# Kernel optimization log

Measured on AMD Instinct MI355X. Metric: run time of the kernel, lower is better.

Reference implementation:

```python
import jax, jax.numpy as jnp
import numpy as np

BS, N, D_IN, HID, D_OUT = 16, 256, 128, 128, 128


def setup_inputs() -> dict:
    key = jax.random.key(0)
    ks = jax.random.split(key, 10)
    s = 0.02
    return {
        "x": jax.random.normal(ks[0], (BS, N, D_IN), dtype=jnp.float32),
        "adj": jax.random.randint(ks[1], (BS, N, N), 0, 2, dtype=jnp.int32),
        "W_fc": jax.random.normal(ks[2], (D_IN, HID), dtype=jnp.float32) * s,
        "b_fc": jnp.zeros((HID,), dtype=jnp.float32),
        "W_a1": jax.random.normal(ks[3], (2 * HID, HID), dtype=jnp.float32) * s,
        "b_a1": jnp.zeros((HID,), dtype=jnp.float32),
        "w_a2": jax.random.normal(ks[4], (HID,), dtype=jnp.float32) * s,
        "b_a2": jnp.zeros((), dtype=jnp.float32),
        "W_out": jax.random.normal(ks[5], (HID, D_OUT), dtype=jnp.float32) * s,
        "b_out": jnp.zeros((D_OUT,), dtype=jnp.float32),
    }


def reference(x, adj, W_fc, b_fc, W_a1, b_a1, w_a2, b_a2, W_out, b_out):
    # h = fc(x): (bs, n, hid)
    h = jnp.einsum("bnd,dh->bnh", x, W_fc) + b_fc
    # attn first layer on concat([h_i, h_j]) decomposes into two half-projections
    # (same math as Linear(2*hid, hid) on the concatenated pair features).
    a_i = jnp.einsum("bnh,hk->bnk", h, W_a1[:HID])  # contribution of h_i
    a_j = jnp.einsum("bnh,hk->bnk", h, W_a1[HID:])  # contribution of h_j
    pre = a_i[:, :, None, :] + a_j[:, None, :, :] + b_a1  # (bs, n, n, hid)
    e = jnp.einsum("bijk,k->bij", jax.nn.relu(pre), w_a2) + b_a2  # (bs, n, n)
    e = jnp.where(adj == 0, jnp.float32(-1e9), e)
    attn = jax.nn.softmax(e, axis=-1)
    h_prime = jnp.einsum("bij,bjh->bih", attn, h)
    out = jnp.einsum("bih,ho->bio", h_prime, W_out) + b_out
    return out
```

## Files before the change

### kernel.cpp

```cpp
#include <hip/hip_runtime.h>

#define BS  16
#define NN  256
#define HID 128

__device__ __forceinline__ int xcd_swz(int bid) {
    return (bid & 7) * 128 + (bid >> 3);
}

__global__ __launch_bounds__(256, 4) void gat_k1(
    const float* __restrict__ x, const float* __restrict__ W_fc,
    const float* __restrict__ b_fc, const float* __restrict__ W_a1,
    const float* __restrict__ b_a1, const float* __restrict__ W_out,
    float* __restrict__ aiT, float* __restrict__ ajT, float* __restrict__ g)
{
    __shared__ __align__(16) float hs[4 * HID];

    const int tid = threadIdx.x;
    const int k   = tid & 127;
    const int q   = tid >> 7;
    const int swz = xcd_swz(blockIdx.x);
    const int r0  = swz * 4;
    const int b   = r0 >> 8;
    const int n0  = r0 & 255;

    const float* x0 = x + __builtin_amdgcn_readfirstlane((r0 + 2 * q) * HID);
    const float* x1 = x0 + HID;

    {
        const float bf = b_fc[k];
        float a0a = bf, a0b = 0.f, a1a = bf, a1b = 0.f;
        #pragma unroll 4
        for (int d0 = 0; d0 < HID; d0 += 8) {
            float w[8];
            #pragma unroll
            for (int t = 0; t < 8; ++t) w[t] = W_fc[(d0 + t) * HID + k];
            a0a += x0[d0+0]*w[0] + x0[d0+1]*w[1] + x0[d0+2]*w[2] + x0[d0+3]*w[3];
            a0b += x0[d0+4]*w[4] + x0[d0+5]*w[5] + x0[d0+6]*w[6] + x0[d0+7]*w[7];
            a1a += x1[d0+0]*w[0] + x1[d0+1]*w[1] + x1[d0+2]*w[2] + x1[d0+3]*w[3];
            a1b += x1[d0+4]*w[4] + x1[d0+5]*w[5] + x1[d0+6]*w[6] + x1[d0+7]*w[7];
        }
        hs[(2 * q + 0) * HID + k] = a0a + a0b;
        hs[(2 * q + 1) * HID + k] = a1a + a1b;
    }
    __syncthreads();

    {
        const float* Wp  = W_a1 + q * HID * HID;
        const float bias = q ? 0.f : b_a1[k];
        float acc[4][2];
        #pragma unroll
        for (int r = 0; r < 4; ++r) { acc[r][0] = bias; acc[r][1] = 0.f; }
        #pragma unroll 2
        for (int d0 = 0; d0 < HID; d0 += 8) {
            float w[8];
            #pragma unroll
            for (int t = 0; t < 8; ++t) w[t] = Wp[(d0 + t) * HID + k];
            #pragma unroll
            for (int r = 0; r < 4; ++r) {
                const float4 h0 = *(const float4*)&hs[r * HID + d0];
                const float4 h1 = *(const float4*)&hs[r * HID + d0 + 4];
                acc[r][0] += h0.x * w[0] + h0.y * w[1] + h0.z * w[2] + h0.w * w[3];
                acc[r][1] += h1.x * w[4] + h1.y * w[5] + h1.z * w[6] + h1.w * w[7];
            }
        }
        float* dst = (q ? ajT : aiT) + (b * HID + k) * NN + n0;
        const float4 v = {acc[0][0] + acc[0][1], acc[1][0] + acc[1][1],
                          acc[2][0] + acc[2][1], acc[3][0] + acc[3][1]};
        *(float4*)dst = v;
    }

    {
        float a0a = 0.f, a0b = 0.f, a1a = 0.f, a1b = 0.f;
        #pragma unroll 4
        for (int d0 = 0; d0 < HID; d0 += 8) {
            float w[8];
            #pragma unroll
            for (int t = 0; t < 8; ++t) w[t] = W_out[(d0 + t) * HID + k];
            const float4 hA0 = *(const float4*)&hs[(2 * q + 0) * HID + d0];
            const float4 hA1 = *(const float4*)&hs[(2 * q + 0) * HID + d0 + 4];
            const float4 hB0 = *(const float4*)&hs[(2 * q + 1) * HID + d0];
            const float4 hB1 = *(const float4*)&hs[(2 * q + 1) * HID + d0 + 4];
            a0a += hA0.x * w[0] + hA0.y * w[1] + hA0.z * w[2] + hA0.w * w[3];
            a0b += hA1.x * w[4] + hA1.y * w[5] + hA1.z * w[6] + hA1.w * w[7];
            a1a += hB0.x * w[0] + hB0.y * w[1] + hB0.z * w[2] + hB0.w * w[3];
            a1b += hB1.x * w[4] + hB1.y * w[5] + hB1.z * w[6] + hB1.w * w[7];
        }
        g[(r0 + 2 * q + 0) * HID + k] = a0a + a0b;
        g[(r0 + 2 * q + 1) * HID + k] = a1a + a1b;
    }
}

__global__ __launch_bounds__(256, 4) void gat_k2(
    const float* __restrict__ aiT, const float* __restrict__ ajT,
    const float* __restrict__ g,  const int* __restrict__ adj,
    const float* __restrict__ w_a2, const float* __restrict__ b_a2,
    const float* __restrict__ b_out, float* __restrict__ out)
{
    __shared__ __align__(16) float ep[4][NN];
    __shared__ __align__(16) float red[2][4][HID];

    const int tid = threadIdx.x;
    const int swz = xcd_swz(blockIdx.x);
    const int b   = swz >> 6;
    const int i0  = (swz & 63) * 4;
    const int wv  = tid >> 6, lane = tid & 63;
    const int j   = wv * 64 + lane;

    int am[4];
    #pragma unroll
    for (int r = 0; r < 4; ++r) am[r] = adj[(b * NN + i0 + r) * NN + j];

    {
        const float* ajp = ajT + b * HID * NN + j;
        const float* aip = aiT + __builtin_amdgcn_readfirstlane(b * HID * NN + i0);
        float acc[4] = {0.f, 0.f, 0.f, 0.f};
        #pragma unroll 8
        for (int kk = 0; kk < HID; ++kk) {
            const float a   = ajp[kk * NN];
            const float4 s4 = *(const float4*)&aip[kk * NN];
            const float wk  = w_a2[kk];
            acc[0] += fmaxf(s4.x + a, 0.f) * wk;
            acc[1] += fmaxf(s4.y + a, 0.f) * wk;
            acc[2] += fmaxf(s4.z + a, 0.f) * wk;
            acc[3] += fmaxf(s4.w + a, 0.f) * wk;
        }
        const float ba2 = b_a2[0];
        #pragma unroll
        for (int r = 0; r < 4; ++r)
            ep[r][j] = am[r] ? acc[r] + ba2 : -1e9f;
    }
    __syncthreads();

    {
        float4 e4 = *(const float4*)&ep[wv][4 * lane];
        float m = fmaxf(fmaxf(e4.x, e4.y), fmaxf(e4.z, e4.w));
        #pragma unroll
        for (int off = 32; off; off >>= 1) m = fmaxf(m, __shfl_xor(m, off));
        const float p0 = __expf(e4.x - m), p1 = __expf(e4.y - m);
        const float p2 = __expf(e4.z - m), p3 = __expf(e4.w - m);
        float s = (p0 + p1) + (p2 + p3);
        #pragma unroll
        for (int off = 32; off; off >>= 1) s += __shfl_xor(s, off);
        const float inv = 1.f / s;
        const float4 pv = {p0 * inv, p1 * inv, p2 * inv, p3 * inv};
        *(float4*)&ep[wv][4 * lane] = pv;
    }
    __syncthreads();

    const int k = tid & 127, qh = tid >> 7;
    {
        float o[4] = {0.f, 0.f, 0.f, 0.f};
        const float* gb = g + (b * NN + qh * 128) * HID + k;
        const int jb = qh * 128;
        #pragma unroll 4
        for (int jq = 0; jq < 128; jq += 4) {
            const float g0 = gb[(jq + 0) * HID];
            const float g1 = gb[(jq + 1) * HID];
            const float g2 = gb[(jq + 2) * HID];
            const float g3 = gb[(jq + 3) * HID];
            const float4 pA = *(const float4*)&ep[0][jb + jq];
            const float4 pB = *(const float4*)&ep[1][jb + jq];
            const float4 pC = *(const float4*)&ep[2][jb + jq];
            const float4 pD = *(const float4*)&ep[3][jb + jq];
            o[0] += pA.x * g0 + pA.y * g1 + pA.z * g2 + pA.w * g3;
            o[1] += pB.x * g0 + pB.y * g1 + pB.z * g2 + pB.w * g3;
            o[2] += pC.x * g0 + pC.y * g1 + pC.z * g2 + pC.w * g3;
            o[3] += pD.x * g0 + pD.y * g1 + pD.z * g2 + pD.w * g3;
        }
        #pragma unroll
        for (int r = 0; r < 4; ++r) red[qh][r][k] = o[r];
    }
    __syncthreads();

    {
        const float bo = b_out[k];
        #pragma unroll
        for (int r2 = 0; r2 < 2; ++r2) {
            const int r = 2 * qh + r2;
            out[(b * NN + i0 + r) * HID + k] =
                red[0][r][k] + red[1][r][k] + bo;
        }
    }
}

extern "C" void kernel_launch(void* const* d_in, const int* in_sizes, int n_in,
                              void* d_out, int out_size, void* d_ws, size_t ws_size,
                              hipStream_t stream) {
    const float* x     = (const float*)d_in[0];
    const int*   adj   = (const int*)  d_in[1];
    const float* W_fc  = (const float*)d_in[2];
    const float* b_fc  = (const float*)d_in[3];
    const float* W_a1  = (const float*)d_in[4];
    const float* b_a1  = (const float*)d_in[5];
    const float* w_a2  = (const float*)d_in[6];
    const float* b_a2  = (const float*)d_in[7];
    const float* W_out = (const float*)d_in[8];
    const float* b_out = (const float*)d_in[9];
    float* out = (float*)d_out;

    float* ws  = (float*)d_ws;
    float* aiT = ws;
    float* ajT = ws + BS * NN * HID;
    float* g   = ws + 2 * BS * NN * HID;

    gat_k1<<<BS * NN / 4, 256, 0, stream>>>(x, W_fc, b_fc, W_a1, b_a1, W_out,
                                            aiT, ajT, g);
    gat_k2<<<BS * (NN / 4), 256, 0, stream>>>(aiT, ajT, g, adj, w_a2, b_a2,
                                              b_out, out);
}
```

Before: 43.88 us.

## Process 8 rows per 512-thread block with split-K smem reductions in both kernels

Both kernels now handle 8 rows per block with 512 threads instead of 4 rows with 256. The goal is to halve the global reads of the weight matrices and the ajT/g tiles per output row. In kernel 1 the x rows are staged in shared memory, and each GEMM is split along the reduction dimension across 4 thread groups, with partial sums combined through a shared-memory reduction buffer. In kernel 2 the aiT slice and w_a2 are staged in shared memory, and the attention-score and aggregation loops are reorganised for 8 rows. The cost is more barriers, more shared memory per block, and a grid half the size, which may reduce the number of waves in flight.

```diff
diff --git a/kernel.cpp b/kernel.cpp
--- a/kernel.cpp
+++ b/kernel.cpp
@@ -5,130 +5,175 @@
 #define HID 128
 
 __device__ __forceinline__ int xcd_swz(int bid) {
-    return (bid & 7) * 128 + (bid >> 3);
-}
-
-__global__ __launch_bounds__(256, 4) void gat_k1(
+    return (bid & 7) * 64 + (bid >> 3);
+}
+
+__global__ __launch_bounds__(512, 4) void gat_k1(
     const float* __restrict__ x, const float* __restrict__ W_fc,
     const float* __restrict__ b_fc, const float* __restrict__ W_a1,
     const float* __restrict__ b_a1, const float* __restrict__ W_out,
     float* __restrict__ aiT, float* __restrict__ ajT, float* __restrict__ g)
 {
-    __shared__ __align__(16) float hs[4 * HID];
+    __shared__ __align__(16) float xs[8][HID];
+    __shared__ __align__(16) float hs[8][HID];
+    __shared__ __align__(16) float red[4][8][HID];
 
     const int tid = threadIdx.x;
     const int k   = tid & 127;
     const int q   = tid >> 7;
     const int swz = xcd_swz(blockIdx.x);
-    const int r0  = swz * 4;
+    const int r0  = swz * 8;
     const int b   = r0 >> 8;
     const int n0  = r0 & 255;
 
-    const float* x0 = x + __builtin_amdgcn_readfirstlane((r0 + 2 * q) * HID);
-    const float* x1 = x0 + HID;
+    for (int t = tid; t < 8 * HID; t += 512)
+        xs[t >> 7][t & 127] = x[r0 * HID + t];
+    __syncthreads();
+
+    {
+        float acc[8] = {0,0,0,0,0,0,0,0};
+        const int dq = 32 * q;
+        #pragma unroll 2
+        for (int d = 0; d < 32; d += 4) {
+            float w[4];
+            #pragma unroll
+            for (int t = 0; t < 4; ++t) w[t] = W_fc[(dq + d + t) * HID + k];
+            #pragma unroll
+            for (int r = 0; r < 8; ++r) {
+                const float4 xv = *(const float4*)&xs[r][dq + d];
+                acc[r] += xv.x * w[0] + xv.y * w[1] + xv.z * w[2] + xv.w * w[3];
+            }
+        }
+        #pragma unroll
+        for (int r = 0; r < 8; ++r) red[q][r][k] = acc[r];
+    }
+    __syncthreads();
 
     {
         const float bf = b_fc[k];
-        float a0a = bf, a0b = 0.f, a1a = bf, a1b = 0.f;
-        #pragma unroll 4
-        for (int d0 = 0; d0 < HID; d0 += 8) {
-            float w[8];
-            #pragma unroll
-            for (int t = 0; t < 8; ++t) w[t] = W_fc[(d0 + t) * HID + k];
-            a0a += x0[d0+0]*w[0] + x0[d0+1]*w[1] + x0[d0+2]*w[2] + x0[d0+3]*w[3];
-            a0b += x0[d0+4]*w[4] + x0[d0+5]*w[5] + x0[d0+6]*w[6] + x0[d0+7]*w[7];
-            a1a += x1[d0+0]*w[0] + x1[d0+1]*w[1] + x1[d0+2]*w[2] + x1[d0+3]*w[3];
-            a1b += x1[d0+4]*w[4] + x1[d0+5]*w[5] + x1[d0+6]*w[6] + x1[d0+7]*w[7];
-        }
-        hs[(2 * q + 0) * HID + k] = a0a + a0b;
-        hs[(2 * q + 1) * HID + k] = a1a + a1b;
-    }
-    __syncthreads();
-
-    {
-        const float* Wp  = W_a1 + q * HID * HID;
-        const float bias = q ? 0.f : b_a1[k];
-        float acc[4][2];
-        #pragma unroll
-        for (int r = 0; r < 4; ++r) { acc[r][0] = bias; acc[r][1] = 0.f; }
-        #pragma unroll 2
-        for (int d0 = 0; d0 < HID; d0 += 8) {
-            float w[8];
-            #pragma unroll
-            for (int t = 0; t < 8; ++t) w[t] = Wp[(d0 + t) * HID + k];
-            #pragma unroll
-            for (int r = 0; r < 4; ++r) {
-                const float4 h0 = *(const float4*)&hs[r * HID + d0];
-                const float4 h1 = *(const float4*)&hs[r * HID + d0 + 4];
-                acc[r][0] += h0.x * w[0] + h0.y * w[1] + h0.z * w[2] + h0.w * w[3];
-                acc[r][1] += h1.x * w[4] + h1.y * w[5] + h1.z * w[6] + h1.w * w[7];
-            }
-        }
-        float* dst = (q ? ajT : aiT) + (b * HID + k) * NN + n0;
-        const float4 v = {acc[0][0] + acc[0][1], acc[1][0] + acc[1][1],
-                          acc[2][0] + acc[2][1], acc[3][0] + acc[3][1]};
+        #pragma unroll
+        for (int r2 = 0; r2 < 2; ++r2) {
+            const int r = 2 * q + r2;
+            hs[r][k] = (red[0][r][k] + red[1][r][k])
+                     + (red[2][r][k] + red[3][r][k]) + bf;
+        }
+    }
+    __syncthreads();
+
+    {
+        const int is_aj = q >> 1;
+        const int half  = q & 1;
+        const float* Wp = W_a1 + (is_aj * HID + half * 64) * HID;
+        float acc[8] = {0,0,0,0,0,0,0,0};
+        const int hb = half * 64;
+        #pragma unroll 2
+        for (int d = 0; d < 64; d += 4) {
+            float w[4];
+            #pragma unroll
+            for (int t = 0; t < 4; ++t) w[t] = Wp[(d + t) * HID + k];
+            #pragma unroll
+            for (int r = 0; r < 8; ++r) {
+                const float4 hv = *(const float4*)&hs[r][hb + d];
+                acc[r] += hv.x * w[0] + hv.y * w[1] + hv.z * w[2] + hv.w * w[3];
+            }
+        }
+        #pragma unroll
+        for (int r = 0; r < 8; ++r) red[q][r][k] = acc[r];
+    }
+    __syncthreads();
+
+    {
+        const int is_aj = q >> 1;
+        const int rb4   = (q & 1) * 4;
+        const float bias = is_aj ? 0.f : b_a1[k];
+        const int p0 = 2 * is_aj, p1 = 2 * is_aj + 1;
+        float4 v;
+        v.x = red[p0][rb4 + 0][k] + red[p1][rb4 + 0][k] + bias;
+        v.y = red[p0][rb4 + 1][k] + red[p1][rb4 + 1][k] + bias;
+        v.z = red[p0][rb4 + 2][k] + red[p1][rb4 + 2][k] + bias;
+        v.w = red[p0][rb4 + 3][k] + red[p1][rb4 + 3][k] + bias;
+        float* dst = (is_aj ? ajT : aiT) + (b * HID + k) * NN + n0 + rb4;
         *(float4*)dst = v;
     }
-
-    {
-        float a0a = 0.f, a0b = 0.f, a1a = 0.f, a1b = 0.f;
-        #pragma unroll 4
-        for (int d0 = 0; d0 < HID; d0 += 8) {
-            float w[8];
-            #pragma unroll
-            for (int t = 0; t < 8; ++t) w[t] = W_out[(d0 + t) * HID + k];
-            const float4 hA0 = *(const float4*)&hs[(2 * q + 0) * HID + d0];
-            const float4 hA1 = *(const float4*)&hs[(2 * q + 0) * HID + d0 + 4];
-            const float4 hB0 = *(const float4*)&hs[(2 * q + 1) * HID + d0];
-            const float4 hB1 = *(const float4*)&hs[(2 * q + 1) * HID + d0 + 4];
-            a0a += hA0.x * w[0] + hA0.y * w[1] + hA0.z * w[2] + hA0.w * w[3];
-            a0b += hA1.x * w[4] + hA1.y * w[5] + hA1.z * w[6] + hA1.w * w[7];
-            a1a += hB0.x * w[0] + hB0.y * w[1] + hB0.z * w[2] + hB0.w * w[3];
-            a1b += hB1.x * w[4] + hB1.y * w[5] + hB1.z * w[6] + hB1.w * w[7];
-        }
-        g[(r0 + 2 * q + 0) * HID + k] = a0a + a0b;
-        g[(r0 + 2 * q + 1) * HID + k] = a1a + a1b;
-    }
-}
-
-__global__ __launch_bounds__(256, 4) void gat_k2(
+    __syncthreads();
+
+    {
+        float acc[8] = {0,0,0,0,0,0,0,0};
+        const int dq = 32 * q;
+        #pragma unroll 2
+        for (int d = 0; d < 32; d += 4) {
+            float w[4];
+            #pragma unroll
+            for (int t = 0; t < 4; ++t) w[t] = W_out[(dq + d + t) * HID + k];
+            #pragma unroll
+            for (int r = 0; r < 8; ++r) {
+                const float4 hv = *(const float4*)&hs[r][dq + d];
+                acc[r] += hv.x * w[0] + hv.y * w[1] + hv.z * w[2] + hv.w * w[3];
+            }
+        }
+        #pragma unroll
+        for (int r = 0; r < 8; ++r) red[q][r][k] = acc[r];
+    }
+    __syncthreads();
+
+    {
+        #pragma unroll
+        for (int r2 = 0; r2 < 2; ++r2) {
+            const int r = 2 * q + r2;
+            g[(r0 + r) * HID + k] = (red[0][r][k] + red[1][r][k])
+                                  + (red[2][r][k] + red[3][r][k]);
+        }
+    }
+}
+
+__global__ __launch_bounds__(512, 4) void gat_k2(
     const float* __restrict__ aiT, const float* __restrict__ ajT,
     const float* __restrict__ g,  const int* __restrict__ adj,
     const float* __restrict__ w_a2, const float* __restrict__ b_a2,
     const float* __restrict__ b_out, float* __restrict__ out)
 {
-    __shared__ __align__(16) float ep[4][NN];
-    __shared__ __align__(16) float red[2][4][HID];
+    __shared__ __align__(16) float aiw[HID][8];
+    __shared__ __align__(16) float w2s[HID];
+    __shared__ __align__(16) float ep[8][NN];
+    __shared__ __align__(16) float red[4][8][HID];
 
     const int tid = threadIdx.x;
     const int swz = xcd_swz(blockIdx.x);
-    const int b   = swz >> 6;
-    const int i0  = (swz & 63) * 4;
+    const int b   = swz >> 5;
+    const int i0  = (swz & 31) * 8;
     const int wv  = tid >> 6, lane = tid & 63;
-    const int j   = wv * 64 + lane;
-
-    int am[4];
-    #pragma unroll
-    for (int r = 0; r < 4; ++r) am[r] = adj[(b * NN + i0 + r) * NN + j];
-
-    {
-        const float* ajp = ajT + b * HID * NN + j;
-        const float* aip = aiT + __builtin_amdgcn_readfirstlane(b * HID * NN + i0);
+
+    for (int t = tid; t < HID * 8; t += 512) {
+        const int kk = t >> 3, r = t & 7;
+        aiw[kk][r] = aiT[(b * HID + kk) * NN + i0 + r];
+    }
+    if (tid < HID) w2s[tid] = w_a2[tid];
+    __syncthreads();
+
+    const int jj = 32 * wv + (lane & 31);
+    const int rg = lane >> 5;
+    {
+        int am[4];
+        #pragma unroll
+        for (int r = 0; r < 4; ++r)
+            am[r] = adj[(b * NN + i0 + 4 * rg + r) * NN + jj];
+
+        const float* ajp = ajT + b * HID * NN + jj;
         float acc[4] = {0.f, 0.f, 0.f, 0.f};
         #pragma unroll 8
         for (int kk = 0; kk < HID; ++kk) {
             const float a   = ajp[kk * NN];
-            const float4 s4 = *(const float4*)&aip[kk * NN];
-            const float wk  = w_a2[kk];
-            acc[0] += fmaxf(s4.x + a, 0.f) * wk;
-            acc[1] += fmaxf(s4.y + a, 0.f) * wk;
-            acc[2] += fmaxf(s4.z + a, 0.f) * wk;
-            acc[3] += fmaxf(s4.w + a, 0.f) * wk;
+            const float4 f4 = *(const float4*)&aiw[kk][4 * rg];
+            const float wk  = w2s[kk];
+            acc[0] += fmaxf(f4.x + a, 0.f) * wk;
+            acc[1] += fmaxf(f4.y + a, 0.f) * wk;
+            acc[2] += fmaxf(f4.z + a, 0.f) * wk;
+            acc[3] += fmaxf(f4.w + a, 0.f) * wk;
         }
         const float ba2 = b_a2[0];
         #pragma unroll
         for (int r = 0; r < 4; ++r)
-            ep[r][j] = am[r] ? acc[r] + ba2 : -1e9f;
+            ep[4 * rg + r][jj] = am[r] ? acc[r] + ba2 : -1e9f;
     }
     __syncthreads();
 
@@ -150,26 +195,23 @@
 
     const int k = tid & 127, qh = tid >> 7;
     {
-        float o[4] = {0.f, 0.f, 0.f, 0.f};
-        const float* gb = g + (b * NN + qh * 128) * HID + k;
-        const int jb = qh * 128;
-        #pragma unroll 4
-        for (int jq = 0; jq < 128; jq += 4) {
+        float o[8] = {0,0,0,0,0,0,0,0};
+        const float* gb = g + (b * NN + qh * 64) * HID + k;
+        const int jb = qh * 64;
+        #pragma unroll 2
+        for (int jq = 0; jq < 64; jq += 4) {
             const float g0 = gb[(jq + 0) * HID];
             const float g1 = gb[(jq + 1) * HID];
             const float g2 = gb[(jq + 2) * HID];
             const float g3 = gb[(jq + 3) * HID];
-            const float4 pA = *(const float4*)&ep[0][jb + jq];
-            const float4 pB = *(const float4*)&ep[1][jb + jq];
-            const float4 pC = *(const float4*)&ep[2][jb + jq];
-            const float4 pD = *(const float4*)&ep[3][jb + jq];
-            o[0] += pA.x * g0 + pA.y * g1 + pA.z * g2 + pA.w * g3;
-            o[1] += pB.x * g0 + pB.y * g1 + pB.z * g2 + pB.w * g3;
-            o[2] += pC.x * g0 + pC.y * g1 + pC.z * g2 + pC.w * g3;
-            o[3] += pD.x * g0 + pD.y * g1 + pD.z * g2 + pD.w * g3;
-        }
-        #pragma unroll
-        for (int r = 0; r < 4; ++r) red[qh][r][k] = o[r];
+            #pragma unroll
+            for (int r = 0; r < 8; ++r) {
+                const float4 pv = *(const float4*)&ep[r][jb + jq];
+                o[r] += pv.x * g0 + pv.y * g1 + pv.z * g2 + pv.w * g3;
+            }
+        }
+        #pragma unroll
+        for (int r = 0; r < 8; ++r) red[qh][r][k] = o[r];
     }
     __syncthreads();
 
@@ -179,7 +221,8 @@
         for (int r2 = 0; r2 < 2; ++r2) {
             const int r = 2 * qh + r2;
             out[(b * NN + i0 + r) * HID + k] =
-                red[0][r][k] + red[1][r][k] + bo;
+                (red[0][r][k] + red[1][r][k]) +
+                (red[2][r][k] + red[3][r][k]) + bo;
         }
     }
 }
@@ -204,8 +247,8 @@
     float* ajT = ws + BS * NN * HID;
     float* g   = ws + 2 * BS * NN * HID;
 
-    gat_k1<<<BS * NN / 4, 256, 0, stream>>>(x, W_fc, b_fc, W_a1, b_a1, W_out,
+    gat_k1<<<BS * NN / 8, 512, 0, stream>>>(x, W_fc, b_fc, W_a1, b_a1, W_out,
                                             aiT, ajT, g);
-    gat_k2<<<BS * (NN / 4), 256, 0, stream>>>(aiT, ajT, g, adj, w_a2, b_a2,
+    gat_k2<<<BS * (NN / 8), 512, 0, stream>>>(aiT, ajT, g, adj, w_a2, b_a2,
                                               b_out, out);
 }
```

Measured after the change: 41.41 us. 5.6% less time.
